# Optimization experiments

Hardware: AMD Instinct MI355X
Metric: run time of the kernel (lower is better)

The kernel has to match this reference:

```python
import jax, jax.numpy as jnp
import numpy as np

B, C, H, W, K = 64, 384, 28, 28, 9
N = H * W
BN_EPS = 1e-5

def _bn(x, g, b, m, v):
    # inference-mode BatchNorm over last (channel) axis
    return (x - m) * (g * jax.lax.rsqrt(v + BN_EPS)) + b

def _gather_nb(x, idx):
    # x [B,N,C], idx [B,N,k] -> neighbor features [B,N,k,C]
    return jax.vmap(lambda xb, ib: xb[ib])(x, idx)

def _gin(x, nb_idx, w, w1, b1, w2, b2, eps):
    # GIN-style conv with per-edge weights w [B,N,k]
    nb = _gather_nb(x, nb_idx)                       # [B,N,k,C]
    agg = jnp.einsum('bnk,bnkc->bnc', w, nb)         # weighted neighbor sum
    h = (1.0 + eps) * x + agg
    return jax.nn.relu(h @ w1 + b1) @ w2 + b2

def setup_inputs():
    key = jax.random.key(0)
    ks = jax.random.split(key, 16)
    rn = lambda i, shape, s=0.05: jax.random.normal(ks[i], shape, jnp.float32) * s
    C4 = 4 * C
    return dict(
        x=jax.random.normal(ks[0], (B, C, H, W), jnp.float32),
        k=K,
        fc1_w=rn(1, (C, C)), fc1_b=jnp.zeros((C,), jnp.float32),
        bn1_g=jnp.ones((C,), jnp.float32), bn1_b=jnp.zeros((C,), jnp.float32),
        bn1_m=rn(2, (C,), 0.1), bn1_v=jax.random.uniform(ks[3], (C,), jnp.float32, 0.5, 1.5),
        gin_eps=jnp.zeros((), jnp.float32),
        gin_w1=rn(4, (C, 2 * C)), gin_b1=jnp.zeros((2 * C,), jnp.float32),
        gin_w2=rn(5, (2 * C, C)), gin_b2=jnp.zeros((C,), jnp.float32),
        att_w1=rn(6, (2 * C, C)), att_b1=jnp.zeros((C,), jnp.float32),
        att_w2=rn(7, (C,)), att_b2=jnp.zeros((), jnp.float32),
        ffn_w1=rn(8, (C, C4)), ffn_b1=jnp.zeros((C4,), jnp.float32),
        fbn1_g=jnp.ones((C4,), jnp.float32), fbn1_b=jnp.zeros((C4,), jnp.float32),
        fbn1_m=rn(9, (C4,), 0.1), fbn1_v=jax.random.uniform(ks[10], (C4,), jnp.float32, 0.5, 1.5),
        ffn_w2=rn(11, (C4, C)), ffn_b2=jnp.zeros((C,), jnp.float32),
        fbn2_g=jnp.ones((C,), jnp.float32), fbn2_b=jnp.zeros((C,), jnp.float32),
        fbn2_m=rn(12, (C,), 0.1), fbn2_v=jax.random.uniform(ks[13], (C,), jnp.float32, 0.5, 1.5),
    )

def reference(x, k, fc1_w, fc1_b, bn1_g, bn1_b, bn1_m, bn1_v, gin_eps,
              gin_w1, gin_b1, gin_w2, gin_b2, att_w1, att_b1, att_w2, att_b2,
              ffn_w1, ffn_b1, fbn1_g, fbn1_b, fbn1_m, fbn1_v,
              ffn_w2, ffn_b2, fbn2_g, fbn2_b, fbn2_m, fbn2_v):
    Bs, Cc, Hh, Ww = x.shape
    Nn = Hh * Ww
    # fc1: 1x1 conv + BatchNorm (channel-last layout [B,N,C])
    h = jnp.transpose(x, (0, 2, 3, 1)).reshape(Bs, Nn, Cc)
    h = _bn(h @ fc1_w.T + fc1_b, bn1_g, bn1_b, bn1_m, bn1_v)
    # L2-normalize node features
    nf = h / jnp.maximum(jnp.linalg.norm(h, axis=-1, keepdims=True), 1e-12)
    # dynamic kNN graph per image (no_grad in original -> stop_gradient indices)
    nfd = jax.lax.stop_gradient(nf)
    sim = jnp.einsum('bnc,bmc->bnm', nfd, nfd)
    sim = sim - 4.0 * jnp.eye(Nn, dtype=sim.dtype)   # exclude self-loops
    nb_idx = jax.lax.top_k(sim, k)[1]                # [B,N,k] nearest neighbors
    # GNN pass 1 (unit edge weights) -> edge-attention extractor
    ones = jnp.ones((Bs, Nn, k), nf.dtype)
    emb = _gin(nf, nb_idx, ones, gin_w1, gin_b1, gin_w2, gin_b2, gin_eps)
    src = _gather_nb(emb, nb_idx)                    # [B,N,k,C]
    dst = jnp.broadcast_to(emb[:, :, None, :], src.shape)
    eh = jax.nn.relu(jnp.concatenate([dst, src], -1) @ att_w1 + att_b1)
    edge_att = jax.nn.sigmoid(eh @ att_w2 + att_b2)  # [B,N,k]
    # GNN pass 2 weighted by the learned edge attention
    ne = _gin(nf, nb_idx, edge_att, gin_w1, gin_b1, gin_w2, gin_b2, gin_eps)
    # ViG FFN: conv1x1+BN -> gelu -> conv1x1+BN -> residual
    y = _bn(ne @ ffn_w1 + ffn_b1, fbn1_g, fbn1_b, fbn1_m, fbn1_v)
    y = jax.nn.gelu(y)
    y = _bn(y @ ffn_w2 + ffn_b2, fbn2_g, fbn2_b, fbn2_m, fbn2_v)
    y = y + ne
    node_embeddings = jnp.transpose(y.reshape(Bs, Hh, Ww, Cc), (0, 3, 1, 2))
    return edge_att.reshape(-1), node_embeddings
```

## Files before the change

### kernel.cpp

```cpp
#include <hip/hip_runtime.h>
#include <math.h>


constexpr int C_  = 384;
constexpr int N_  = 784;
constexpr int B_  = 64;
constexpr int R_  = B_ * N_;
constexpr int E_  = R_ * 9;
constexpr long RC_ = (long)R_ * C_;
constexpr int NT_ = 13;
constexpr int NC_ = NT_ * 9;

typedef __bf16 bf16_t;
typedef __attribute__((ext_vector_type(8))) __bf16 bf16x8;
typedef __attribute__((ext_vector_type(4))) float f32x4;

__device__ __forceinline__ float gelu_tanh(float x) {
    float x3 = x * x * x;
    return 0.5f * x * (1.0f + tanhf(0.7978845608028654f * (x + 0.044715f * x3)));
}

__global__ void prep_bn(const float* __restrict__ g1, const float* __restrict__ v1,
                        const float* __restrict__ gf1, const float* __restrict__ bf1,
                        const float* __restrict__ mf1, const float* __restrict__ vf1,
                        const float* __restrict__ gf2, const float* __restrict__ bf2,
                        const float* __restrict__ mf2, const float* __restrict__ vf2,
                        float* __restrict__ prep) {
    int i = blockIdx.x * 256 + threadIdx.x;
    float* pB1s = prep;
    float* pF1s = prep + 768;  float* pF1t = prep + 2304;
    float* pF2s = prep + 3840; float* pF2t = prep + 4224;
    if (i < 1536) {
        float s = gf1[i] * rsqrtf(vf1[i] + 1e-5f);
        pF1s[i] = s; pF1t[i] = bf1[i] - mf1[i] * s;
    }
    if (i < 384) {
        const float inv = __fdiv_rn(1.0f, sqrtf(__fadd_rn(v1[i], 1e-5f)));
        pB1s[i] = __fmul_rn(g1[i], inv);
        float s = gf2[i] * rsqrtf(vf2[i] + 1e-5f);
        pF2s[i] = s; pF2t[i] = bf2[i] - mf2[i] * s;
    }
}

__global__ void wconv_T(const float* __restrict__ W, bf16_t* __restrict__ WT,
                        int K, int N) {
    const int idx = blockIdx.x * 256 + threadIdx.x;
    if (idx >= N * K) return;
    const int n = idx / K, k = idx - n * K;
    WT[idx] = (bf16_t)W[(size_t)k * N + n];
}

__global__ __launch_bounds__(256) void fc1_gemm(
    const float* __restrict__ x, const float* __restrict__ fw,
    const float* __restrict__ fb, const float* __restrict__ s1,
    const float* __restrict__ m1, const float* __restrict__ bb1,
    float* __restrict__ out) {
    __shared__ float As[16][68];
    __shared__ float Bs[16][68];
    const int m0 = blockIdx.x * 64, o0 = blockIdx.y * 64;
    const int tid = threadIdx.x;
    const int tx = tid & 15, ty = tid >> 4;
    const int lm = tid & 63, kk = tid >> 6;
    const int gm = m0 + lm, bb = gm / N_, nn = gm - bb * N_;
    const float* xp = x + (size_t)bb * C_ * N_ + nn;
    const int lo = tid >> 2, lk = (tid & 3) * 4;
    const float* wp = fw + (size_t)(o0 + lo) * C_ + lk;
    float acc[4][4] = {};
    for (int k0 = 0; k0 < C_; k0 += 16) {
        float xa[4];
#pragma unroll
        for (int j = 0; j < 4; ++j) xa[j] = xp[(size_t)(k0 + kk * 4 + j) * N_];
        float4 wv = *(const float4*)(wp + k0);
#pragma unroll
        for (int j = 0; j < 4; ++j) As[kk * 4 + j][lm] = xa[j];
        Bs[lk + 0][lo] = wv.x; Bs[lk + 1][lo] = wv.y;
        Bs[lk + 2][lo] = wv.z; Bs[lk + 3][lo] = wv.w;
        __syncthreads();
#pragma unroll
        for (int k = 0; k < 16; ++k) {
            const float4 a4 = *(const float4*)&As[k][ty * 4];
            const float4 b4 = *(const float4*)&Bs[k][tx * 4];
            const float a[4] = {a4.x, a4.y, a4.z, a4.w};
            const float bq[4] = {b4.x, b4.y, b4.z, b4.w};
#pragma unroll
            for (int i = 0; i < 4; ++i)
#pragma unroll
                for (int j = 0; j < 4; ++j)
                    acc[i][j] = fmaf(a[i], bq[j], acc[i][j]);
        }
        __syncthreads();
    }
#pragma unroll
    for (int i = 0; i < 4; ++i) {
        const int m = m0 + ty * 4 + i;
        float* cp = out + (size_t)m * C_ + o0 + tx * 4;
        float4 o; float* ov = (float*)&o;
#pragma unroll
        for (int j = 0; j < 4; ++j) {
            const int n = o0 + tx * 4 + j;
            const float z = __fadd_rn(acc[i][j], fb[n]);
            const float u = __fsub_rn(z, m1[n]);
            ov[j] = __fadd_rn(__fmul_rn(u, s1[n]), bb1[n]);
        }
        *(float4*)cp = o;
    }
}

__global__ __launch_bounds__(256) void rownorm_np(const float* __restrict__ h,
                                                  float* __restrict__ nm) {
    const int row = blockIdx.x * 256 + threadIdx.x;
    if (row >= R_) return;
    const float* p = h + (size_t)row * C_;
    float Bv[4];
#pragma unroll
    for (int b4 = 0; b4 < 4; ++b4) {
        const float* a = p + b4 * 96;
        float r[8];
#pragma unroll
        for (int j = 0; j < 8; ++j) r[j] = __fmul_rn(a[j], a[j]);
        for (int i = 8; i < 96; i += 8) {
#pragma unroll
            for (int j = 0; j < 8; ++j)
                r[j] = __fadd_rn(r[j], __fmul_rn(a[i + j], a[i + j]));
        }
        Bv[b4] = __fadd_rn(
            __fadd_rn(__fadd_rn(r[0], r[1]), __fadd_rn(r[2], r[3])),
            __fadd_rn(__fadd_rn(r[4], r[5]), __fadd_rn(r[6], r[7])));
    }
    const float s = __fadd_rn(__fadd_rn(Bv[0], Bv[1]), __fadd_rn(Bv[2], Bv[3]));
    nm[row] = fmaxf(sqrtf(s), 1e-12f);
}

__global__ __launch_bounds__(256) void l2div(float* __restrict__ h,
                                             const float* __restrict__ nm) {
    const int row = blockIdx.x * 4 + (threadIdx.x >> 6);
    const int lane = threadIdx.x & 63;
    const float d = nm[row];
    float* p = h + (size_t)row * C_;
#pragma unroll
    for (int t = 0; t < 6; ++t) p[lane + 64 * t] = __fdiv_rn(p[lane + 64 * t], d);
}

__global__ __launch_bounds__(256) void sim_topk_np(
    const float* __restrict__ nf, float* __restrict__ cv, int* __restrict__ ci) {
    __shared__ float As[16][68];
    __shared__ float Bs[16][68];
    const int n0 = blockIdx.x * 64, m0 = blockIdx.y * 64, b = blockIdx.z;
    const float* nfb = nf + (size_t)b * N_ * C_;
    const int tid = threadIdx.x;
    const int tx = tid & 15, ty = tid >> 4;
    const int lr = tid >> 2, lk = (tid & 3) * 4;
    const bool va = (n0 + lr) < N_;
    const bool vb = (m0 + lr) < N_;
    const float* pa = nfb + (size_t)(n0 + lr) * C_ + lk;
    const float* pb = nfb + (size_t)(m0 + lr) * C_ + lk;
    float acc[4][4][4] = {};
    for (int k0 = 0; k0 < C_; k0 += 16) {
        float4 av = {0.f, 0.f, 0.f, 0.f}, bv = {0.f, 0.f, 0.f, 0.f};
        if (va) av = *(const float4*)(pa + k0);
        if (vb) bv = *(const float4*)(pb + k0);
        As[lk + 0][lr] = av.x; As[lk + 1][lr] = av.y;
        As[lk + 2][lr] = av.z; As[lk + 3][lr] = av.w;
        Bs[lk + 0][lr] = bv.x; Bs[lk + 1][lr] = bv.y;
        Bs[lk + 2][lr] = bv.z; Bs[lk + 3][lr] = bv.w;
        __syncthreads();
#pragma unroll
        for (int grp = 0; grp < 4; ++grp) {
            const int kb = (3 - grp) * 4;
#pragma unroll
            for (int kl = 0; kl < 4; ++kl) {
                const int k = kb + kl;
                const float4 a4 = *(const float4*)&As[k][ty * 4];
                const float4 b4 = *(const float4*)&Bs[k][tx * 4];
                const float a[4] = {a4.x, a4.y, a4.z, a4.w};
                const float bq[4] = {b4.x, b4.y, b4.z, b4.w};
#pragma unroll
                for (int i = 0; i < 4; ++i)
#pragma unroll
                    for (int j = 0; j < 4; ++j)
                        acc[i][j][kl] = __fadd_rn(__fmul_rn(a[i], bq[j]),
                                                  acc[i][j][kl]);
            }
        }
        __syncthreads();
    }
#pragma unroll
    for (int i = 0; i < 4; ++i) {
        const int n = n0 + ty * 4 + i;
        float sv[4]; int si[4];
#pragma unroll
        for (int j = 0; j < 4; ++j) {
            const float* r = acc[i][j];
            float v = __fadd_rn(__fadd_rn(r[0], r[1]), __fadd_rn(r[2], r[3]));
            const int m = m0 + tx * 4 + j;
            if (n == m) v = __fsub_rn(v, 4.0f);
            if (m >= N_) v = -3.0e38f;
            sv[j] = v; si[j] = m;
        }
#pragma unroll
        for (int s = 0; s < 5; ++s) {
            const int pa_[5] = {0, 2, 0, 1, 1};
            const int pb_[5] = {1, 3, 2, 3, 2};
            const int a_ = pa_[s], b_ = pb_[s];
            const bool sw = (sv[b_] > sv[a_]) || (sv[b_] == sv[a_] && si[b_] < si[a_]);
            const float tv = sw ? sv[b_] : sv[a_]; const int ti = sw ? si[b_] : si[a_];
            sv[b_] = sw ? sv[a_] : sv[b_]; si[b_] = sw ? si[a_] : si[b_];
            sv[a_] = tv; si[a_] = ti;
        }
#pragma unroll
        for (int it = 0; it < 9; ++it) {
            float bv2 = sv[0]; int bi = si[0];
#pragma unroll
            for (int mk = 1; mk <= 8; mk <<= 1) {
                const float ov = __shfl_xor(bv2, mk, 64);
                const int  oi = __shfl_xor(bi, mk, 64);
                if (ov > bv2 || (ov == bv2 && oi < bi)) { bv2 = ov; bi = oi; }
            }
            if (si[0] == bi) {
                sv[0] = sv[1]; si[0] = si[1];
                sv[1] = sv[2]; si[1] = si[2];
                sv[2] = sv[3]; si[2] = si[3];
                sv[3] = -3.0e38f; si[3] = 0x7fffffff;
            }
            if (tx == 0 && n < N_) {
                const size_t o = ((size_t)b * N_ + n) * NC_ + blockIdx.y * 9 + it;
                cv[o] = bv2; ci[o] = bi;
            }
        }
    }
}

__global__ __launch_bounds__(256) void merge_topk(
    const float* __restrict__ cv, const int* __restrict__ ci,
    int* __restrict__ nbidx) {
    const int row = blockIdx.x * 4 + (threadIdx.x >> 6);
    const int lane = threadIdx.x & 63;
    const size_t base = (size_t)row * NC_;
    float v0 = cv[base + lane]; int i0 = ci[base + lane];
    float v1 = -3.0e38f; int i1 = 0x7fffffff;
    if (lane + 64 < NC_) { v1 = cv[base + 64 + lane]; i1 = ci[base + 64 + lane]; }
#pragma unroll
    for (int it = 0; it < 9; ++it) {
        float bv = v0; int bi = i0;
        if (v1 > bv || (v1 == bv && i1 < bi)) { bv = v1; bi = i1; }
#pragma unroll
        for (int off = 32; off; off >>= 1) {
            const float ov = __shfl_xor(bv, off, 64);
            const int  oi = __shfl_xor(bi, off, 64);
            if (ov > bv || (ov == bv && oi < bi)) { bv = ov; bi = oi; }
        }
        if (i0 == bi) v0 = -3.0e38f;
        if (i1 == bi) v1 = -3.0e38f;
        if (lane == 0) nbidx[(size_t)row * 9 + it] = bi;
    }
}

__global__ void gin_gather(const float* __restrict__ nf, const int* __restrict__ nbidx,
                           const float* __restrict__ w, const float* __restrict__ epsp,
                           bf16_t* __restrict__ outbf) {
    const int node = blockIdx.x;
    const int c = threadIdx.x;
    const int b = node / N_;
    const float* nfb = nf + (size_t)b * N_ * C_;
    const int nl = node - b * N_;
    float acc = (1.0f + epsp[0]) * nfb[(size_t)nl * C_ + c];
#pragma unroll
    for (int j = 0; j < 9; ++j) {
        const int ij = nbidx[(size_t)node * 9 + j];
        const float wj = w ? w[(size_t)node * 9 + j] : 1.0f;
        acc += wj * nfb[(size_t)ij * C_ + c];
    }
    outbf[(size_t)node * C_ + c] = (bf16_t)acc;
}

template <int ACT, bool ACCUM, bool WF32, bool WBF>
__global__ __launch_bounds__(256) void bgemm(
    const bf16_t* __restrict__ A, int lda, int ka,
    const bf16_t* __restrict__ WT, int ldwt,
    const float* __restrict__ bias, const float* __restrict__ bns,
    const float* __restrict__ bnt,
    float* __restrict__ Cf, bf16_t* __restrict__ Cb, int ldc) {
    const int wave = threadIdx.x >> 6, lane = threadIdx.x & 63;
    const int m0 = blockIdx.x * 128 + wave * 32;
    const int n0 = blockIdx.y * 64;
    const int csub = lane & 15;
    const int kslot = (lane >> 4) * 8;
    const bf16_t* ap0 = A + (size_t)(m0 + csub) * lda + kslot;
    const bf16_t* ap1 = A + (size_t)(m0 + 16 + csub) * lda + kslot;
    f32x4 acc[2][4];
#pragma unroll
    for (int mi = 0; mi < 2; ++mi)
#pragma unroll
        for (int c4 = 0; c4 < 4; ++c4) acc[mi][c4] = (f32x4){0.f, 0.f, 0.f, 0.f};
    const bf16_t* bp[4];
#pragma unroll
    for (int c4 = 0; c4 < 4; ++c4)
        bp[c4] = WT + (size_t)(n0 + c4 * 16 + csub) * ldwt + kslot;
    for (int k0 = 0; k0 < ka; k0 += 32) {
        const bf16x8 a0 = *(const bf16x8*)(ap0 + k0);
        const bf16x8 a1 = *(const bf16x8*)(ap1 + k0);
#pragma unroll
        for (int c4 = 0; c4 < 4; ++c4) {
            const bf16x8 bfrag = *(const bf16x8*)(bp[c4] + k0);
            acc[0][c4] = __builtin_amdgcn_mfma_f32_16x16x32_bf16(a0, bfrag, acc[0][c4], 0, 0, 0);
            acc[1][c4] = __builtin_amdgcn_mfma_f32_16x16x32_bf16(a1, bfrag, acc[1][c4], 0, 0, 0);
        }
    }
#pragma unroll
    for (int mi = 0; mi < 2; ++mi) {
        const int rbase = m0 + mi * 16 + (lane >> 4) * 4;
#pragma unroll
        for (int c4 = 0; c4 < 4; ++c4) {
            const int gcol = n0 + c4 * 16 + csub;
#pragma unroll
            for (int r = 0; r < 4; ++r) {
                const int grow = rbase + r;
                float z = acc[mi][c4][r];
                if (bias) z += bias[gcol];
                if (bns)  z = z * bns[gcol] + bnt[gcol];
                if (ACT == 1) z = fmaxf(z, 0.0f);
                if (ACT == 2) z = gelu_tanh(z);
                if (ACCUM) z += Cf[(size_t)grow * ldc + gcol];
                if (WF32) Cf[(size_t)grow * ldc + gcol] = z;
                if (WBF)  Cb[(size_t)grow * ldc + gcol] = (bf16_t)z;
            }
        }
    }
}

__global__ __launch_bounds__(256) void edge_att_node(
    const float* __restrict__ eA, const float* __restrict__ eB,
    const int* __restrict__ nbidx, const float* __restrict__ w2,
    const float* __restrict__ b2p, float* __restrict__ out) {
    const int node = blockIdx.x * 4 + (threadIdx.x >> 6);
    const int lane = threadIdx.x & 63;
    const int b = node / N_;
    const float* pa = eA + (size_t)node * C_;
    const float* ebb = eB + (size_t)b * N_ * C_;
    int idx[9];
#pragma unroll
    for (int j = 0; j < 9; ++j) idx[j] = nbidx[(size_t)node * 9 + j];
    float s[9];
#pragma unroll
    for (int j = 0; j < 9; ++j) s[j] = 0.f;
#pragma unroll
    for (int t = 0; t < 6; ++t) {
        const int c = lane + 64 * t;
        const float a = pa[c];
        const float w = w2[c];
#pragma unroll
        for (int j = 0; j < 9; ++j)
            s[j] += fmaxf(a + ebb[(size_t)idx[j] * C_ + c], 0.f) * w;
    }
#pragma unroll
    for (int j = 0; j < 9; ++j)
#pragma unroll
        for (int off = 32; off; off >>= 1) s[j] += __shfl_xor(s[j], off, 64);
    if (lane < 9)
        out[(size_t)node * 9 + lane] =
            1.0f / (1.0f + expf(-(s[lane] + b2p[0])));
}

__global__ __launch_bounds__(256) void ffn_final(
    const float* __restrict__ acc, const float* __restrict__ ne,
    const float* __restrict__ b2, const float* __restrict__ s2,
    const float* __restrict__ t2, float* __restrict__ out) {
    __shared__ float T[32][33];
    const int bb = blockIdx.z;
    const int n0 = blockIdx.x * 32, c0 = blockIdx.y * 32;
    const int tx = threadIdx.x, ty = threadIdx.y;
#pragma unroll
    for (int ii = 0; ii < 4; ++ii) {
        const int nl = ty + 8 * ii;
        const int n = n0 + nl, c = c0 + tx;
        float z = 0.f;
        if (n < N_) {
            const size_t o = ((size_t)bb * N_ + n) * C_ + c;
            z = (acc[o] + b2[c]) * s2[c] + t2[c] + ne[o];
        }
        T[nl][tx] = z;
    }
    __syncthreads();
#pragma unroll
    for (int ii = 0; ii < 4; ++ii) {
        const int cl = ty + 8 * ii;
        const int n = n0 + tx;
        if (n < N_) out[((size_t)bb * C_ + c0 + cl) * N_ + n] = T[tx][cl];
    }
}

extern "C" void kernel_launch(void* const* d_in, const int* in_sizes, int n_in,
                              void* d_out, int out_size, void* d_ws, size_t ws_size,
                              hipStream_t stream) {
    (void)in_sizes; (void)n_in; (void)out_size; (void)ws_size;
    const float* x      = (const float*)d_in[0];
    const float* fc1_w  = (const float*)d_in[2];
    const float* fc1_b  = (const float*)d_in[3];
    const float* bn1_g  = (const float*)d_in[4];
    const float* bn1_b  = (const float*)d_in[5];
    const float* bn1_m  = (const float*)d_in[6];
    const float* bn1_v  = (const float*)d_in[7];
    const float* gineps = (const float*)d_in[8];
    const float* gin_w1 = (const float*)d_in[9];
    const float* gin_b1 = (const float*)d_in[10];
    const float* gin_w2 = (const float*)d_in[11];
    const float* gin_b2 = (const float*)d_in[12];
    const float* att_w1 = (const float*)d_in[13];
    const float* att_b1 = (const float*)d_in[14];
    const float* att_w2 = (const float*)d_in[15];
    const float* att_b2 = (const float*)d_in[16];
    const float* ffn_w1 = (const float*)d_in[17];
    const float* ffn_b1 = (const float*)d_in[18];
    const float* fbn1_g = (const float*)d_in[19];
    const float* fbn1_b = (const float*)d_in[20];
    const float* fbn1_m = (const float*)d_in[21];
    const float* fbn1_v = (const float*)d_in[22];
    const float* ffn_w2 = (const float*)d_in[23];
    const float* ffn_b2 = (const float*)d_in[24];
    const float* fbn2_g = (const float*)d_in[25];
    const float* fbn2_b = (const float*)d_in[26];
    const float* fbn2_m = (const float*)d_in[27];
    const float* fbn2_v = (const float*)d_in[28];

    float* outp = (float*)d_out;

    float* P0 = (float*)d_ws;
    float* P1 = P0 + RC_;
    float* P2 = P0 + 2 * RC_;
    int*   nbidx = (int*)(P0 + 3 * RC_);
    float* prep  = (float*)(nbidx + E_);
    float* norms = prep + 4608;
    bf16_t* gw1T = (bf16_t*)(norms + R_);
    bf16_t* gw2T = gw1T + 768 * 384;
    bf16_t* fw1T = gw2T + 384 * 768;
    bf16_t* fw2T = fw1T + 1536 * 384;
    bf16_t* aw1Ttop = fw2T + 384 * 1536;
    bf16_t* aw1Tbot = aw1Ttop + 384 * 384;
    float* cv = P0;
    int*   ci = (int*)(cv + (size_t)R_ * NC_);
    float* EMB = outp + E_;
    const float* pB1s = prep;
    const float* pF1s = prep + 768,  *pF1t = prep + 2304;
    const float* pF2s = prep + 3840, *pF2t = prep + 4224;

    const dim3 gg6(784, 6), gb6(392, 6), gb12(392, 12);

    prep_bn<<<6, 256, 0, stream>>>(bn1_g, bn1_v,
                                   fbn1_g, fbn1_b, fbn1_m, fbn1_v,
                                   fbn2_g, fbn2_b, fbn2_m, fbn2_v, prep);
    wconv_T<<<(768 * 384 + 255) / 256, 256, 0, stream>>>(gin_w1, gw1T, 384, 768);
    wconv_T<<<(384 * 768 + 255) / 256, 256, 0, stream>>>(gin_w2, gw2T, 768, 384);
    wconv_T<<<(1536 * 384 + 255) / 256, 256, 0, stream>>>(ffn_w1, fw1T, 384, 1536);
    wconv_T<<<(384 * 1536 + 255) / 256, 256, 0, stream>>>(ffn_w2, fw2T, 1536, 384);
    wconv_T<<<(384 * 384 + 255) / 256, 256, 0, stream>>>(att_w1, aw1Ttop, 384, 384);
    wconv_T<<<(384 * 384 + 255) / 256, 256, 0, stream>>>(att_w1 + (size_t)384 * 384,
                                                         aw1Tbot, 384, 384);

    fc1_gemm<<<gg6, 256, 0, stream>>>(x, fc1_w, fc1_b, pB1s, bn1_m, bn1_b, P2);
    rownorm_np<<<R_ / 256, 256, 0, stream>>>(P2, norms);
    l2div<<<R_ / 4, 256, 0, stream>>>(P2, norms);
    sim_topk_np<<<dim3(NT_, NT_, B_), 256, 0, stream>>>(P2, cv, ci);
    merge_topk<<<R_ / 4, 256, 0, stream>>>(cv, ci, nbidx);

    bf16_t* h1bf  = (bf16_t*)P0;
    bf16_t* midbf = (bf16_t*)P1;
    bf16_t* embbf = (bf16_t*)(P0 + RC_ / 2);
    gin_gather<<<R_, 384, 0, stream>>>(P2, nbidx, nullptr, gineps, h1bf);
    bgemm<1, false, false, true><<<gb12, 256, 0, stream>>>(
        h1bf, 384, 384, gw1T, 384, gin_b1, nullptr, nullptr,
        nullptr, midbf, 768);
    bgemm<0, false, false, true><<<gb6, 256, 0, stream>>>(
        midbf, 768, 768, gw2T, 768, gin_b2, nullptr, nullptr,
        nullptr, embbf, 384);

    bgemm<0, false, true, false><<<gb6, 256, 0, stream>>>(
        embbf, 384, 384, aw1Ttop, 384, att_b1, nullptr, nullptr,
        P1, nullptr, 384);
    bgemm<0, false, true, false><<<gb6, 256, 0, stream>>>(
        embbf, 384, 384, aw1Tbot, 384, nullptr, nullptr, nullptr,
        EMB, nullptr, 384);
    edge_att_node<<<R_ / 4, 256, 0, stream>>>(P1, EMB, nbidx, att_w2, att_b2, outp);

    bf16_t* h2bf = (bf16_t*)P0;
    bf16_t* nebf = (bf16_t*)EMB;
    gin_gather<<<R_, 384, 0, stream>>>(P2, nbidx, outp, gineps, h2bf);
    bgemm<1, false, false, true><<<gb12, 256, 0, stream>>>(
        h2bf, 384, 384, gw1T, 384, gin_b1, nullptr, nullptr,
        nullptr, (bf16_t*)P1, 768);
    bgemm<0, false, true, true><<<gb6, 256, 0, stream>>>(
        (bf16_t*)P1, 768, 768, gw2T, 768, gin_b2, nullptr, nullptr,
        P0, nebf, 384);

    bf16_t* ybf = (bf16_t*)P1;
    for (int g = 0; g < 2; ++g) {
        bgemm<2, false, false, true><<<gb12, 256, 0, stream>>>(
            nebf, 384, 384, fw1T + (size_t)g * 768 * 384, 384,
            ffn_b1 + g * 768, pF1s + g * 768, pF1t + g * 768,
            nullptr, ybf, 768);
        if (g == 0)
            bgemm<0, false, true, false><<<gb6, 256, 0, stream>>>(
                ybf, 768, 768, fw2T + (size_t)g * 768, 1536,
                nullptr, nullptr, nullptr, P2, nullptr, 384);
        else
            bgemm<0, true, true, false><<<gb6, 256, 0, stream>>>(
                ybf, 768, 768, fw2T + (size_t)g * 768, 1536,
                nullptr, nullptr, nullptr, P2, nullptr, 384);
    }

    ffn_final<<<dim3(25, 12, 64), dim3(32, 8), 0, stream>>>(P2, P0, ffn_b2,
                                                            pF2s, pF2t, outp + E_);
}
```

Baseline: 2.911 ms.

## Exploit similarity-matrix symmetry by computing only upper-triangular tiles in top-k

The similarity GEMM now launches only upper-triangular 64x64 tile pairs per batch, since nf·nfᵀ is symmetric. Each off-diagonal tile writes row-wise top-9 candidates for its n rows as before. It then transposes the tile through shared memory and computes column-wise top-9 candidates for the m rows with wave shuffles. This roughly halves the fp32 GEMM work, at the cost of an extra transpose and a second selection pass on off-diagonal tiles.

Result: slower. 3.216 ms (+10.5%).

```diff
diff --git a/kernel.cpp b/kernel.cpp
--- a/kernel.cpp
+++ b/kernel.cpp
@@ -10,6 +10,7 @@
 constexpr long RC_ = (long)R_ * C_;
 constexpr int NT_ = 13;
 constexpr int NC_ = NT_ * 9;
+constexpr int NTRI_ = NT_ * (NT_ + 1) / 2;
 
 typedef __bf16 bf16_t;
 typedef __attribute__((ext_vector_type(8))) __bf16 bf16x8;
@@ -143,9 +144,14 @@
 
 __global__ __launch_bounds__(256) void sim_topk_np(
     const float* __restrict__ nf, float* __restrict__ cv, int* __restrict__ ci) {
-    __shared__ float As[16][68];
-    __shared__ float Bs[16][68];
-    const int n0 = blockIdx.x * 64, m0 = blockIdx.y * 64, b = blockIdx.z;
+    __shared__ float smem[4160];
+    float (*As)[68] = (float(*)[68])smem;
+    float (*Bs)[68] = (float(*)[68])(smem + 16 * 68);
+    float (*T)[65]  = (float(*)[65])smem;
+    int t = blockIdx.x, bx = 0;
+    while (t >= NT_ - bx) { t -= NT_ - bx; ++bx; }
+    const int by = bx + t;
+    const int n0 = bx * 64, m0 = by * 64, b = blockIdx.z;
     const float* nfb = nf + (size_t)b * N_ * C_;
     const int tid = threadIdx.x;
     const int tx = tid & 15, ty = tid >> 4;
@@ -184,10 +190,10 @@
         }
         __syncthreads();
     }
+    float fin[4][4];
 #pragma unroll
     for (int i = 0; i < 4; ++i) {
         const int n = n0 + ty * 4 + i;
-        float sv[4]; int si[4];
 #pragma unroll
         for (int j = 0; j < 4; ++j) {
             const float* r = acc[i][j];
@@ -195,8 +201,15 @@
             const int m = m0 + tx * 4 + j;
             if (n == m) v = __fsub_rn(v, 4.0f);
             if (m >= N_) v = -3.0e38f;
-            sv[j] = v; si[j] = m;
-        }
+            fin[i][j] = v;
+        }
+    }
+#pragma unroll
+    for (int i = 0; i < 4; ++i) {
+        const int n = n0 + ty * 4 + i;
+        float sv[4]; int si[4];
+#pragma unroll
+        for (int j = 0; j < 4; ++j) { sv[j] = fin[i][j]; si[j] = m0 + tx * 4 + j; }
 #pragma unroll
         for (int s = 0; s < 5; ++s) {
             const int pa_[5] = {0, 2, 0, 1, 1};
@@ -223,7 +236,38 @@
                 sv[3] = -3.0e38f; si[3] = 0x7fffffff;
             }
             if (tx == 0 && n < N_) {
-                const size_t o = ((size_t)b * N_ + n) * NC_ + blockIdx.y * 9 + it;
+                const size_t o = ((size_t)b * N_ + n) * NC_ + by * 9 + it;
+                cv[o] = bv2; ci[o] = bi;
+            }
+        }
+    }
+    if (bx == by) return;
+    __syncthreads();
+#pragma unroll
+    for (int i = 0; i < 4; ++i)
+#pragma unroll
+        for (int j = 0; j < 4; ++j)
+            T[tx * 4 + j][ty * 4 + i] = fin[i][j];
+    __syncthreads();
+    const int wv = tid >> 6, lane = tid & 63;
+    for (int rr = 0; rr < 16; ++rr) {
+        const int r = wv * 16 + rr;
+        const int m = m0 + r;
+        if (m >= N_) continue;
+        float val = T[r][lane];
+        int idx = n0 + lane;
+#pragma unroll
+        for (int it = 0; it < 9; ++it) {
+            float bv2 = val; int bi = idx;
+#pragma unroll
+            for (int off = 32; off; off >>= 1) {
+                const float ov = __shfl_xor(bv2, off, 64);
+                const int  oi = __shfl_xor(bi, off, 64);
+                if (ov > bv2 || (ov == bv2 && oi < bi)) { bv2 = ov; bi = oi; }
+            }
+            if (idx == bi) val = -3.0e38f;
+            if (lane == 0) {
+                const size_t o = ((size_t)b * N_ + m) * NC_ + bx * 9 + it;
                 cv[o] = bv2; ci[o] = bi;
             }
         }
@@ -459,7 +503,7 @@
     fc1_gemm<<<gg6, 256, 0, stream>>>(x, fc1_w, fc1_b, pB1s, bn1_m, bn1_b, P2);
     rownorm_np<<<R_ / 256, 256, 0, stream>>>(P2, norms);
     l2div<<<R_ / 4, 256, 0, stream>>>(P2, norms);
-    sim_topk_np<<<dim3(NT_, NT_, B_), 256, 0, stream>>>(P2, cv, ci);
+    sim_topk_np<<<dim3(NTRI_, 1, B_), 256, 0, stream>>>(P2, cv, ci);
     merge_topk<<<R_ / 4, 256, 0, stream>>>(cv, ci, nbidx);
 
     bf16_t* h1bf  = (bf16_t*)P0;
```
